# Optimization experiments

Hardware: AMD Instinct MI355X
Metric: run time of the kernel (lower is better)

The kernel has to match this reference:

```python
import jax, jax.numpy as jnp
import numpy as np

B, S, D = 2, 2048, 1024
H = 16
HD = D // H  # 64


def setup_inputs() -> dict:
    key = jax.random.key(0)
    ks = jax.random.split(key, 6)
    std = 1.0 / np.sqrt(D)
    x = jax.random.normal(ks[0], (B, S, D), dtype=jnp.float32)
    Wq = jax.random.uniform(ks[1], (D, D), jnp.float32, -std, std)
    Wk = jax.random.uniform(ks[2], (D, D), jnp.float32, -std, std)
    Wv = jax.random.uniform(ks[3], (D, D), jnp.float32, -std, std)
    Wo = jax.random.uniform(ks[4], (D, D), jnp.float32, -std, std)
    bo = jax.random.uniform(ks[5], (D,), jnp.float32, -std, std)
    return {"x": x, "Wq": Wq, "Wk": Wk, "Wv": Wv, "Wo": Wo, "bo": bo}


def reference(x, Wq, Wk, Wv, Wo, bo):
    b, n, _ = x.shape
    # project and split heads: [b, H, n, HD]
    def split_heads(y):
        return y.reshape(b, n, H, HD).transpose(0, 2, 1, 3)
    q = split_heads(jnp.einsum('bnd,ed->bne', x, Wq))
    k = split_heads(jnp.einsum('bnd,ed->bne', x, Wk))
    v = split_heads(jnp.einsum('bnd,ed->bne', x, Wv))
    scores = jnp.einsum('bhqd,bhkd->bhqk', q, k)
    causal = jnp.triu(jnp.ones((n, n), dtype=bool), k=1)
    # original masks with -inf BEFORE scaling; -inf/scale == -inf so math matches
    scores = jnp.where(causal, -jnp.inf, scores) / jnp.sqrt(jnp.asarray(HD, scores.dtype))
    attn = jax.nn.softmax(scores, axis=-1)
    ctx = jnp.einsum('bhqk,bhkd->bhqd', attn, v)
    ctx = ctx.transpose(0, 2, 1, 3).reshape(b, n, D)
    return jnp.einsum('bnd,ed->bne', ctx, Wo) + bo
```

## Files before the change

### kernel.cpp

```cpp
#include <hip/hip_runtime.h>

#define DEV __device__ __forceinline__

typedef __bf16 bf16x8 __attribute__((ext_vector_type(8)));
typedef float f32x4 __attribute__((ext_vector_type(4)));
typedef float f32x16 __attribute__((ext_vector_type(16)));
typedef unsigned u32x4 __attribute__((ext_vector_type(4)));

constexpr int S_LEN = 2048;
constexpr int DMODEL = 1024;
constexpr int NHEAD = 16;
constexpr int HDIM = 64;
constexpr int BATCH = 2;
constexpr int MROWS = BATCH * S_LEN;
constexpr float QSCALE = 0.125f * 1.44269504088896f;

DEV short f2bf(float x) {
  unsigned u = __builtin_bit_cast(unsigned, x);
  unsigned r = u + 0x7fffu + ((u >> 16) & 1u);
  return (short)(r >> 16);
}

#define MFMA16(a, b, c) __builtin_amdgcn_mfma_f32_16x16x32_bf16((a), (b), (c), 0, 0, 0)
#define MFMA32(a, b, c) __builtin_amdgcn_mfma_f32_32x32x16_bf16((a), (b), (c), 0, 0, 0)
#define GLL16(g, l)                                                                     \
  __builtin_amdgcn_global_load_lds((const __attribute__((address_space(1))) void*)(g),  \
                                   (__attribute__((address_space(3))) void*)(l), 16, 0, 0)

DEV unsigned cvt_pk_bf16(float a, float b) {
  unsigned r;
  asm("v_cvt_pk_bf16_f32 %0, %1, %2" : "=v"(r) : "v"(a), "v"(b));
  return r;
}
DEV void swap32(unsigned& a, unsigned& b) {
  asm("v_permlane32_swap_b32 %0, %1" : "+v"(a), "+v"(b));
}

__global__ void cvt_kernel(const float* __restrict__ in, short* __restrict__ out, int n) {
  int i = (blockIdx.x * blockDim.x + threadIdx.x) * 4;
  const int stride = gridDim.x * blockDim.x * 4;
  for (; i < n; i += stride) {
    float4 v = *(const float4*)&in[i];
    short4 r;
    r.x = f2bf(v.x);
    r.y = f2bf(v.y);
    r.z = f2bf(v.z);
    r.w = f2bf(v.w);
    *(short4*)&out[i] = r;
  }
}

__global__ void cvt_w4(const float* __restrict__ Wq, const float* __restrict__ Wk,
                       const float* __restrict__ Wv, const float* __restrict__ Wo,
                       short* __restrict__ out) {
  const float* src = blockIdx.y == 0 ? Wq : blockIdx.y == 1 ? Wk : blockIdx.y == 2 ? Wv : Wo;
  short* dst = out + (size_t)blockIdx.y * (DMODEL * DMODEL);
  int i = (blockIdx.x * blockDim.x + threadIdx.x) * 4;
  const int stride = gridDim.x * blockDim.x * 4;
  for (; i < DMODEL * DMODEL; i += stride) {
    float4 v = *(const float4*)&src[i];
    short4 r;
    r.x = f2bf(v.x);
    r.y = f2bf(v.y);
    r.z = f2bf(v.z);
    r.w = f2bf(v.w);
    *(short4*)&dst[i] = r;
  }
}

__global__ __launch_bounds__(256) void gemm_bt(const short* __restrict__ A,
                                               const short* __restrict__ Bt,
                                               short* __restrict__ outb) {
  constexpr int K = DMODEL;
  constexpr size_t XN = (size_t)MROWS * DMODEL;
  __shared__ short As[2][128 * 64];
  __shared__ short Bs[2][128 * 64];
  const int tid = threadIdx.x;
  const int w = tid >> 6, l = tid & 63;
  const int lr = l & 15, lh = l >> 4;
  const int wr = w >> 1, wc = w & 1;
  const int tm = blockIdx.x, tn = blockIdx.y;
  const bool vswap = (tn >= 16);

  const int srow = tid >> 3;
  const int ssl = tid & 7;
  const int ssg = ssl ^ (srow & 7);

  f32x4 acc[4][4] = {};

#define GSTAGE(KT, BUF)                                                             \
  {                                                                                 \
    _Pragma("unroll") for (int i = 0; i < 4; ++i) {                                 \
      const int row = i * 32 + srow;                                                \
      GLL16(A + (size_t)(tm * 128 + row) * K + (KT)*64 + ssg * 8,                   \
            &As[BUF][(i * 256 + w * 64) * 8]);                                      \
    }                                                                               \
    _Pragma("unroll") for (int i = 0; i < 4; ++i) {                                 \
      const int row = i * 32 + srow;                                                \
      GLL16(Bt + (size_t)(tn * 128 + row) * K + (KT)*64 + ssg * 8,                  \
            &Bs[BUF][(i * 256 + w * 64) * 8]);                                      \
    }                                                                               \
  }

  GSTAGE(0, 0);
  asm volatile("s_waitcnt vmcnt(0)" ::: "memory");
  __syncthreads();

  for (int kt = 0; kt < K / 64; ++kt) {
    const int buf = kt & 1;
    if (kt < K / 64 - 1) GSTAGE(kt + 1, buf ^ 1);

#pragma unroll
    for (int kh = 0; kh < 2; ++kh) {
      bf16x8 af[4], bfr[4];
#pragma unroll
      for (int mi = 0; mi < 4; ++mi) {
        const int row = wr * 64 + mi * 16 + lr;
        af[mi] = *(const bf16x8*)&As[buf][row * 64 + 8 * ((kh * 4 + lh) ^ (row & 7))];
      }
#pragma unroll
      for (int ni = 0; ni < 4; ++ni) {
        const int row = wc * 64 + ni * 16 + lr;
        bfr[ni] = *(const bf16x8*)&Bs[buf][row * 64 + 8 * ((kh * 4 + lh) ^ (row & 7))];
      }
      if (vswap) {
#pragma unroll
        for (int mi = 0; mi < 4; ++mi)
#pragma unroll
          for (int ni = 0; ni < 4; ++ni)
            acc[mi][ni] = MFMA16(bfr[ni], af[mi], acc[mi][ni]);
      } else {
#pragma unroll
        for (int mi = 0; mi < 4; ++mi)
#pragma unroll
          for (int ni = 0; ni < 4; ++ni)
            acc[mi][ni] = MFMA16(af[mi], bfr[ni], acc[mi][ni]);
      }
    }

    asm volatile("s_waitcnt vmcnt(0)" ::: "memory");
    __syncthreads();
  }
#undef GSTAGE

  const int m0 = tm * 128 + wr * 64;
  const int n0 = tn * 128 + wc * 64;
  if (vswap) {
#pragma unroll
    for (int mi = 0; mi < 4; ++mi)
#pragma unroll
      for (int ni = 0; ni < 4; ++ni)
#pragma unroll
        for (int i = 0; i < 4; ++i) {
          const int e = n0 + ni * 16 + lh * 4 + i;
          const int m = m0 + mi * 16 + lr;
          const int ecol = e & (DMODEL - 1);
          const int b = m >> 11, n = m & (S_LEN - 1);
          const int h = ecol >> 6, d = ecol & (HDIM - 1);
          (outb + 2 * XN)[((size_t)((b * NHEAD + h) * HDIM + d)) * S_LEN + n] =
              f2bf(acc[mi][ni][i]);
        }
  } else {
    const int sel = tn >> 3;
#pragma unroll
    for (int mi = 0; mi < 4; ++mi)
#pragma unroll
      for (int ni = 0; ni < 4; ++ni)
#pragma unroll
        for (int i = 0; i < 4; ++i) {
          const int m = m0 + mi * 16 + lh * 4 + i;
          const int e = n0 + ni * 16 + lr;
          const int ecol = e & (DMODEL - 1);
          const int b = m >> 11, n = m & (S_LEN - 1);
          const int h = ecol >> 6, d = ecol & (HDIM - 1);
          if (sel == 0)
            outb[((size_t)((b * NHEAD + h) * S_LEN + n)) * HDIM + d] =
                f2bf(acc[mi][ni][i] * QSCALE);
          else
            (outb + XN)[((size_t)((b * NHEAD + h) * S_LEN + n)) * HDIM + d] =
                f2bf(acc[mi][ni][i]);
        }
  }
}

__global__ __launch_bounds__(256) void gemm_out(const short* __restrict__ A,
                                                const short* __restrict__ Bt,
                                                float* __restrict__ outf,
                                                const float* __restrict__ bias) {
  constexpr int K = DMODEL;
  constexpr int N = DMODEL;
  __shared__ short As[2][64 * 64];
  __shared__ short Bs[2][128 * 64];
  const int tid = threadIdx.x;
  const int w = tid >> 6, l = tid & 63;
  const int lr = l & 15, lh = l >> 4;
  const int wc = w;
  const int tm = blockIdx.x, tn = blockIdx.y;

  const int srow = tid >> 3;
  const int ssl = tid & 7;
  const int ssg = ssl ^ (srow & 7);

  f32x4 acc[4][2] = {};

#define OSTAGE(KT, BUF)                                                             \
  {                                                                                 \
    _Pragma("unroll") for (int i = 0; i < 2; ++i) {                                 \
      const int row = i * 32 + srow;                                                \
      GLL16(A + (size_t)(tm * 64 + row) * K + (KT)*64 + ssg * 8,                    \
            &As[BUF][(i * 256 + w * 64) * 8]);                                      \
    }                                                                               \
    _Pragma("unroll") for (int i = 0; i < 4; ++i) {                                 \
      const int row = i * 32 + srow;                                                \
      GLL16(Bt + (size_t)(tn * 128 + row) * K + (KT)*64 + ssg * 8,                  \
            &Bs[BUF][(i * 256 + w * 64) * 8]);                                      \
    }                                                                               \
  }

  OSTAGE(0, 0);
  asm volatile("s_waitcnt vmcnt(0)" ::: "memory");
  __syncthreads();

  for (int kt = 0; kt < K / 64; ++kt) {
    const int buf = kt & 1;
    if (kt < K / 64 - 1) OSTAGE(kt + 1, buf ^ 1);

#pragma unroll
    for (int kh = 0; kh < 2; ++kh) {
      bf16x8 af[4], bfr[2];
#pragma unroll
      for (int mi = 0; mi < 4; ++mi) {
        const int row = mi * 16 + lr;
        af[mi] = *(const bf16x8*)&As[buf][row * 64 + 8 * ((kh * 4 + lh) ^ (row & 7))];
      }
#pragma unroll
      for (int ni = 0; ni < 2; ++ni) {
        const int row = wc * 32 + ni * 16 + lr;
        bfr[ni] = *(const bf16x8*)&Bs[buf][row * 64 + 8 * ((kh * 4 + lh) ^ (row & 7))];
      }
#pragma unroll
      for (int mi = 0; mi < 4; ++mi)
#pragma unroll
        for (int ni = 0; ni < 2; ++ni)
          acc[mi][ni] = MFMA16(af[mi], bfr[ni], acc[mi][ni]);
    }

    asm volatile("s_waitcnt vmcnt(0)" ::: "memory");
    __syncthreads();
  }
#undef OSTAGE

#pragma unroll
  for (int mi = 0; mi < 4; ++mi)
#pragma unroll
    for (int ni = 0; ni < 2; ++ni)
#pragma unroll
      for (int i = 0; i < 4; ++i) {
        const int m = tm * 64 + mi * 16 + lh * 4 + i;
        const int e = tn * 128 + wc * 32 + ni * 16 + lr;
        outf[(size_t)m * N + e] = acc[mi][ni][i] + bias[e];
      }
}

__global__ __launch_bounds__(256) void attn_kernel(const short* __restrict__ Qg,
                                                   const short* __restrict__ Kg,
                                                   const short* __restrict__ Vg,
                                                   short* __restrict__ ctx) {
  __shared__ alignas(16) short KV[4][8192];
  __shared__ float mls[4][2][32];
  const int tidx = threadIdx.x;
  const int s = tidx >> 6;
  const int l = tidx & 63;
  const int lq = l & 31;
  const int h5 = l >> 5;
  const int bid = blockIdx.x;
  const int xcd = bid & 7;
  const int j = bid >> 3;
  const int bh = xcd * 4 + (j >> 5);
  const int qc = 31 - (j & 31);
  const int qbase = qc * 64;
  const short* Qh = Qg + (size_t)bh * (S_LEN * HDIM);
  const short* Kh = Kg + (size_t)bh * (S_LEN * HDIM);
  const short* Vh = Vg + (size_t)bh * (HDIM * S_LEN);

  short* Kbase = &KV[s][0];
  short* Vbase = &KV[s][4096];
  const int r8 = l >> 3;
  const int sc = l & 7;

  bf16x8 qf0[4], qf1[4];
#pragma unroll
  for (int cc = 0; cc < 4; ++cc) {
    qf0[cc] = *(const bf16x8*)&Qh[(size_t)(qbase + lq) * HDIM + cc * 16 + h5 * 8];
    qf1[cc] = *(const bf16x8*)&Qh[(size_t)(qbase + 32 + lq) * HDIM + cc * 16 + h5 * 8];
  }

  f32x16 o00 = {}, o01 = {}, o10 = {}, o11 = {};
  float ll0 = 0.f, ll1 = 0.f;

  const int ntot = 2 * qc + 2;
  const int td0 = 2 * qc, td1 = 2 * qc + 1;
  const int ts = (ntot * s) >> 2;
  const int te = (ntot * (s + 1)) >> 2;

#define STAGE(T, BUF)                                                              \
  {                                                                                \
    _Pragma("unroll") for (int i = 0; i < 4; ++i) {                                \
      const int R = i * 8 + r8;                                                    \
      const int sg = sc ^ (R & 7);                                                 \
      GLL16(Kh + (size_t)((T)*32 + R) * HDIM + sg * 8,                             \
            &Kbase[(BUF)*2048 + i * 512]);                                         \
      GLL16(Vh + (size_t)(2 * R + (sg >> 2)) * S_LEN + (T)*32 + (sg & 3) * 8,      \
            &Vbase[(BUF)*2048 + i * 512]);                                         \
    }                                                                              \
  }

  if (ts < te) STAGE(ts, 0);

  for (int t = ts; t < te; ++t) {
    const int buf = (t - ts) & 1;
    if (t + 1 < te) {
      STAGE(t + 1, buf ^ 1);
      asm volatile("s_waitcnt vmcnt(8)" ::: "memory");
    } else {
      asm volatile("s_waitcnt vmcnt(0)" ::: "memory");
    }
    const short* Ksb = &Kbase[buf * 2048];
    const short* Vsb = &Vbase[buf * 2048];

    bf16x8 kf[4];
#pragma unroll
    for (int cc = 0; cc < 4; ++cc)
      kf[cc] = *(const bf16x8*)&Ksb[lq * 64 + 8 * ((cc * 2 + h5) ^ (lq & 7))];
    const int R0 = lq >> 1, p0 = (lq & 1) * 4 + h5;
    const int R1 = 16 + (lq >> 1);
    const bf16x8 v00 = *(const bf16x8*)&Vsb[R0 * 64 + 8 * ((p0 + 0) ^ (R0 & 7))];
    const bf16x8 v01 = *(const bf16x8*)&Vsb[R0 * 64 + 8 * ((p0 + 2) ^ (R0 & 7))];
    const bf16x8 v10 = *(const bf16x8*)&Vsb[R1 * 64 + 8 * ((p0 + 0) ^ (R1 & 7))];
    const bf16x8 v11 = *(const bf16x8*)&Vsb[R1 * 64 + 8 * ((p0 + 2) ^ (R1 & 7))];

    if (t != td1) {
      f32x16 st = {};
      __builtin_amdgcn_s_setprio(1);
#pragma unroll
      for (int cc = 0; cc < 4; ++cc) st = MFMA32(kf[cc], qf0[cc], st);
      __builtin_amdgcn_s_setprio(0);
      if (t == td0) {
#pragma unroll
        for (int rr = 0; rr < 16; ++rr) {
          const int crow = (rr & 3) + 8 * (rr >> 2) + 4 * h5;
          if (crow > lq) st[rr] = -__builtin_inff();
        }
      }
#pragma unroll
      for (int rr = 0; rr < 16; ++rr) {
        st[rr] = __builtin_amdgcn_exp2f(st[rr]);
        ll0 += st[rr];
      }
      unsigned a0 = cvt_pk_bf16(st[0], st[1]), b0 = cvt_pk_bf16(st[4], st[5]);
      unsigned a1 = cvt_pk_bf16(st[2], st[3]), b1 = cvt_pk_bf16(st[6], st[7]);
      unsigned a2 = cvt_pk_bf16(st[8], st[9]), b2 = cvt_pk_bf16(st[12], st[13]);
      unsigned a3 = cvt_pk_bf16(st[10], st[11]), b3 = cvt_pk_bf16(st[14], st[15]);
      swap32(a0, b0);
      swap32(a1, b1);
      swap32(a2, b2);
      swap32(a3, b3);
      const u32x4 pw0 = {a0, a1, b0, b1};
      const u32x4 pw1 = {a2, a3, b2, b3};
      const bf16x8 pa0 = __builtin_bit_cast(bf16x8, pw0);
      const bf16x8 pa1 = __builtin_bit_cast(bf16x8, pw1);
      __builtin_amdgcn_s_setprio(1);
      o00 = MFMA32(pa0, v00, o00);
      o01 = MFMA32(pa0, v10, o01);
      o00 = MFMA32(pa1, v01, o00);
      o01 = MFMA32(pa1, v11, o01);
      __builtin_amdgcn_s_setprio(0);
    }

    {
      f32x16 st = {};
      __builtin_amdgcn_s_setprio(1);
#pragma unroll
      for (int cc = 0; cc < 4; ++cc) st = MFMA32(kf[cc], qf1[cc], st);
      __builtin_amdgcn_s_setprio(0);
      if (t == td1) {
#pragma unroll
        for (int rr = 0; rr < 16; ++rr) {
          const int crow = (rr & 3) + 8 * (rr >> 2) + 4 * h5;
          if (crow > lq) st[rr] = -__builtin_inff();
        }
      }
#pragma unroll
      for (int rr = 0; rr < 16; ++rr) {
        st[rr] = __builtin_amdgcn_exp2f(st[rr]);
        ll1 += st[rr];
      }
      unsigned a0 = cvt_pk_bf16(st[0], st[1]), b0 = cvt_pk_bf16(st[4], st[5]);
      unsigned a1 = cvt_pk_bf16(st[2], st[3]), b1 = cvt_pk_bf16(st[6], st[7]);
      unsigned a2 = cvt_pk_bf16(st[8], st[9]), b2 = cvt_pk_bf16(st[12], st[13]);
      unsigned a3 = cvt_pk_bf16(st[10], st[11]), b3 = cvt_pk_bf16(st[14], st[15]);
      swap32(a0, b0);
      swap32(a1, b1);
      swap32(a2, b2);
      swap32(a3, b3);
      const u32x4 pw0 = {a0, a1, b0, b1};
      const u32x4 pw1 = {a2, a3, b2, b3};
      const bf16x8 pa0 = __builtin_bit_cast(bf16x8, pw0);
      const bf16x8 pa1 = __builtin_bit_cast(bf16x8, pw1);
      __builtin_amdgcn_s_setprio(1);
      o10 = MFMA32(pa0, v00, o10);
      o11 = MFMA32(pa0, v10, o11);
      o10 = MFMA32(pa1, v01, o10);
      o11 = MFMA32(pa1, v11, o11);
      __builtin_amdgcn_s_setprio(0);
    }
  }
#undef STAGE

  float* me = (float*)&KV[s][0];
#pragma unroll
  for (int rr = 0; rr < 16; ++rr) {
    const int crow = (rr & 3) + 8 * (rr >> 2) + 4 * h5;
    me[crow * 64 + lq] = o00[rr];
    me[crow * 64 + 32 + lq] = o01[rr];
    me[(32 + crow) * 64 + lq] = o10[rr];
    me[(32 + crow) * 64 + 32 + lq] = o11[rr];
  }
  ll0 += __shfl_xor(ll0, 32);
  ll1 += __shfl_xor(ll1, 32);
  if (h5 == 0) {
    mls[s][0][lq] = ll0;
    mls[s][1][lq] = ll1;
  }
  __syncthreads();

  const float* om = (const float*)&KV[0][0];
  const int b = bh >> 4, h = bh & (NHEAD - 1);
  const int r2 = tidx >> 2;
  const int d0 = (tidx & 3) * 16;
  const float lsum = mls[0][r2 >> 5][r2 & 31] + mls[1][r2 >> 5][r2 & 31] +
                     mls[2][r2 >> 5][r2 & 31] + mls[3][r2 >> 5][r2 & 31];
  const float inv = __builtin_amdgcn_rcpf(lsum);
  const size_t base = (size_t)(b * S_LEN + qbase + r2) * DMODEL + h * HDIM + d0;
#pragma unroll
  for (int i = 0; i < 16; ++i) {
    const int o = r2 * 64 + d0 + i;
    const float v = om[o] + om[4096 + o] + om[8192 + o] + om[12288 + o];
    ctx[base + i] = f2bf(v * inv);
  }
}

extern "C" void kernel_launch(void* const* d_in, const int* in_sizes, int n_in,
                              void* d_out, int out_size, void* d_ws, size_t ws_size,
                              hipStream_t stream) {
  const float* x = (const float*)d_in[0];
  const float* Wq = (const float*)d_in[1];
  const float* Wk = (const float*)d_in[2];
  const float* Wv = (const float*)d_in[3];
  const float* Wo = (const float*)d_in[4];
  const float* bo = (const float*)d_in[5];

  const size_t XN = (size_t)MROWS * DMODEL;
  const size_t WN = (size_t)DMODEL * DMODEL;

  short* ws = (short*)d_ws;
  short* xb = ws;
  short* Wqb = xb + XN;
  short* Wob = Wqb + 3 * WN;
  short* Qb = Wob + WN;
  short* Kb = Qb + XN;
  short* Vb = Kb + XN;
  short* ctxb = Vb + XN;
  if (ws_size < (5 * XN + 4 * WN) * sizeof(short)) return;

  cvt_kernel<<<2048, 256, 0, stream>>>(x, xb, (int)XN);
  cvt_w4<<<dim3(256, 4), 256, 0, stream>>>(Wq, Wk, Wv, Wo, Wqb);

  gemm_bt<<<dim3(MROWS / 128, 3 * DMODEL / 128), 256, 0, stream>>>(xb, Wqb, Qb);

  attn_kernel<<<1024, 256, 0, stream>>>(Qb, Kb, Vb, ctxb);

  gemm_out<<<dim3(MROWS / 64, DMODEL / 128), 256, 0, stream>>>(ctxb, Wob, (float*)d_out,
                                                               bo);
}
```

Before: 118.4 us.

## Merge conversion kernels, shrink output GEMM tile, tree-reduce softmax row sums

Combines the input and weight bf16 conversions into one launch covering x followed by the four weight matrices, which is contiguous with the existing workspace layout. Changes the output projection GEMM from 64x128 to 64x64 tiles with a 2x2 wave layout, doubling the grid to 1024 blocks for better CU occupancy at the cost of more A-tile reloads. Replaces the serial accumulation of exp values in attention with a pairwise tree sum to shorten the dependency chain.

New measurement: 115.1 us. 1.03x faster.

```diff
diff --git a/kernel.cpp b/kernel.cpp
--- a/kernel.cpp
+++ b/kernel.cpp
@@ -36,35 +36,33 @@
   asm("v_permlane32_swap_b32 %0, %1" : "+v"(a), "+v"(b));
 }
 
-__global__ void cvt_kernel(const float* __restrict__ in, short* __restrict__ out, int n) {
-  int i = (blockIdx.x * blockDim.x + threadIdx.x) * 4;
-  const int stride = gridDim.x * blockDim.x * 4;
-  for (; i < n; i += stride) {
-    float4 v = *(const float4*)&in[i];
+__global__ void cvt_all(const float* __restrict__ x, const float* __restrict__ wq,
+                        const float* __restrict__ wk, const float* __restrict__ wv,
+                        const float* __restrict__ wo, short* __restrict__ out) {
+  const size_t XNe = (size_t)MROWS * DMODEL;
+  const size_t WNe = (size_t)DMODEL * DMODEL;
+  const size_t tot = XNe + 4 * WNe;
+  size_t i = ((size_t)blockIdx.x * blockDim.x + threadIdx.x) * 4;
+  const size_t stride = (size_t)gridDim.x * blockDim.x * 4;
+  for (; i < tot; i += stride) {
+    const float* src;
+    size_t off;
+    if (i < XNe) {
+      src = x;
+      off = i;
+    } else {
+      const size_t k = i - XNe;
+      const int seg = (int)(k >> 20);
+      off = k & (WNe - 1);
+      src = seg == 0 ? wq : seg == 1 ? wk : seg == 2 ? wv : wo;
+    }
+    float4 v = *(const float4*)&src[off];
     short4 r;
     r.x = f2bf(v.x);
     r.y = f2bf(v.y);
     r.z = f2bf(v.z);
     r.w = f2bf(v.w);
     *(short4*)&out[i] = r;
-  }
-}
-
-__global__ void cvt_w4(const float* __restrict__ Wq, const float* __restrict__ Wk,
-                       const float* __restrict__ Wv, const float* __restrict__ Wo,
-                       short* __restrict__ out) {
-  const float* src = blockIdx.y == 0 ? Wq : blockIdx.y == 1 ? Wk : blockIdx.y == 2 ? Wv : Wo;
-  short* dst = out + (size_t)blockIdx.y * (DMODEL * DMODEL);
-  int i = (blockIdx.x * blockDim.x + threadIdx.x) * 4;
-  const int stride = gridDim.x * blockDim.x * 4;
-  for (; i < DMODEL * DMODEL; i += stride) {
-    float4 v = *(const float4*)&src[i];
-    short4 r;
-    r.x = f2bf(v.x);
-    r.y = f2bf(v.y);
-    r.z = f2bf(v.z);
-    r.w = f2bf(v.w);
-    *(short4*)&dst[i] = r;
   }
 }
 
@@ -190,18 +188,18 @@
   constexpr int K = DMODEL;
   constexpr int N = DMODEL;
   __shared__ short As[2][64 * 64];
-  __shared__ short Bs[2][128 * 64];
+  __shared__ short Bs[2][64 * 64];
   const int tid = threadIdx.x;
   const int w = tid >> 6, l = tid & 63;
   const int lr = l & 15, lh = l >> 4;
-  const int wc = w;
+  const int wr = w >> 1, wc = w & 1;
   const int tm = blockIdx.x, tn = blockIdx.y;
 
   const int srow = tid >> 3;
   const int ssl = tid & 7;
   const int ssg = ssl ^ (srow & 7);
 
-  f32x4 acc[4][2] = {};
+  f32x4 acc[2][2] = {};
 
 #define OSTAGE(KT, BUF)                                                             \
   {                                                                                 \
@@ -210,9 +208,9 @@
       GLL16(A + (size_t)(tm * 64 + row) * K + (KT)*64 + ssg * 8,                    \
             &As[BUF][(i * 256 + w * 64) * 8]);                                      \
     }                                                                               \
-    _Pragma("unroll") for (int i = 0; i < 4; ++i) {                                 \
+    _Pragma("unroll") for (int i = 0; i < 2; ++i) {                                 \
       const int row = i * 32 + srow;                                                \
-      GLL16(Bt + (size_t)(tn * 128 + row) * K + (KT)*64 + ssg * 8,                  \
+      GLL16(Bt + (size_t)(tn * 64 + row) * K + (KT)*64 + ssg * 8,                   \
             &Bs[BUF][(i * 256 + w * 64) * 8]);                                      \
     }                                                                               \
   }
@@ -227,10 +225,10 @@
 
 #pragma unroll
     for (int kh = 0; kh < 2; ++kh) {
-      bf16x8 af[4], bfr[2];
-#pragma unroll
-      for (int mi = 0; mi < 4; ++mi) {
-        const int row = mi * 16 + lr;
+      bf16x8 af[2], bfr[2];
+#pragma unroll
+      for (int mi = 0; mi < 2; ++mi) {
+        const int row = wr * 32 + mi * 16 + lr;
         af[mi] = *(const bf16x8*)&As[buf][row * 64 + 8 * ((kh * 4 + lh) ^ (row & 7))];
       }
 #pragma unroll
@@ -239,7 +237,7 @@
         bfr[ni] = *(const bf16x8*)&Bs[buf][row * 64 + 8 * ((kh * 4 + lh) ^ (row & 7))];
       }
 #pragma unroll
-      for (int mi = 0; mi < 4; ++mi)
+      for (int mi = 0; mi < 2; ++mi)
 #pragma unroll
         for (int ni = 0; ni < 2; ++ni)
           acc[mi][ni] = MFMA16(af[mi], bfr[ni], acc[mi][ni]);
@@ -251,13 +249,13 @@
 #undef OSTAGE
 
 #pragma unroll
-  for (int mi = 0; mi < 4; ++mi)
+  for (int mi = 0; mi < 2; ++mi)
 #pragma unroll
     for (int ni = 0; ni < 2; ++ni)
 #pragma unroll
-      for (int i = 0; i < 4; ++i) {
-        const int m = tm * 64 + mi * 16 + lh * 4 + i;
-        const int e = tn * 128 + wc * 32 + ni * 16 + lr;
+      for (int i = 0; i < 2 * 2; ++i) {
+        const int m = tm * 64 + wr * 32 + mi * 16 + lh * 4 + i;
+        const int e = tn * 64 + wc * 32 + ni * 16 + lr;
         outf[(size_t)m * N + e] = acc[mi][ni][i] + bias[e];
       }
 }
@@ -353,9 +351,13 @@
         }
       }
 #pragma unroll
-      for (int rr = 0; rr < 16; ++rr) {
-        st[rr] = __builtin_amdgcn_exp2f(st[rr]);
-        ll0 += st[rr];
+      for (int rr = 0; rr < 16; ++rr) st[rr] = __builtin_amdgcn_exp2f(st[rr]);
+      {
+        const float a = ((st[0] + st[1]) + (st[2] + st[3])) +
+                        ((st[4] + st[5]) + (st[6] + st[7]));
+        const float b = ((st[8] + st[9]) + (st[10] + st[11])) +
+                        ((st[12] + st[13]) + (st[14] + st[15]));
+        ll0 += a + b;
       }
       unsigned a0 = cvt_pk_bf16(st[0], st[1]), b0 = cvt_pk_bf16(st[4], st[5]);
       unsigned a1 = cvt_pk_bf16(st[2], st[3]), b1 = cvt_pk_bf16(st[6], st[7]);
@@ -391,9 +393,13 @@
         }
       }
 #pragma unroll
-      for (int rr = 0; rr < 16; ++rr) {
-        st[rr] = __builtin_amdgcn_exp2f(st[rr]);
-        ll1 += st[rr];
+      for (int rr = 0; rr < 16; ++rr) st[rr] = __builtin_amdgcn_exp2f(st[rr]);
+      {
+        const float a = ((st[0] + st[1]) + (st[2] + st[3])) +
+                        ((st[4] + st[5]) + (st[6] + st[7]));
+        const float b = ((st[8] + st[9]) + (st[10] + st[11])) +
+                        ((st[12] + st[13]) + (st[14] + st[15]));
+        ll1 += a + b;
       }
       unsigned a0 = cvt_pk_bf16(st[0], st[1]), b0 = cvt_pk_bf16(st[4], st[5]);
       unsigned a1 = cvt_pk_bf16(st[2], st[3]), b1 = cvt_pk_bf16(st[6], st[7]);
@@ -473,13 +479,12 @@
   short* ctxb = Vb + XN;
   if (ws_size < (5 * XN + 4 * WN) * sizeof(short)) return;
 
-  cvt_kernel<<<2048, 256, 0, stream>>>(x, xb, (int)XN);
-  cvt_w4<<<dim3(256, 4), 256, 0, stream>>>(Wq, Wk, Wv, Wo, Wqb);
+  cvt_all<<<2048, 256, 0, stream>>>(x, Wq, Wk, Wv, Wo, xb);
 
   gemm_bt<<<dim3(MROWS / 128, 3 * DMODEL / 128), 256, 0, stream>>>(xb, Wqb, Qb);
 
   attn_kernel<<<1024, 256, 0, stream>>>(Qb, Kb, Vb, ctxb);
 
-  gemm_out<<<dim3(MROWS / 64, DMODEL / 128), 256, 0, stream>>>(ctxb, Wob, (float*)d_out,
-                                                               bo);
-}
+  gemm_out<<<dim3(MROWS / 64, DMODEL / 64), 256, 0, stream>>>(ctxb, Wob, (float*)d_out,
+                                                              bo);
+}
```
